# Kernel optimization log

Hardware: AMD Instinct MI355X
Metric: run time of the kernel (lower is better)

## Reference

```python
import jax, jax.numpy as jnp
import numpy as np

HEADS = 16

def _layernorm_LC(x, eps=1e-05):
    # Normalizes jointly over the last TWO dims (L, C), matching the custom LayerNorm.
    mean = jnp.mean(x, axis=(-2, -1), keepdims=True)
    var = jnp.mean((x - mean) ** 2, axis=(-2, -1), keepdims=True) + eps
    return (x - mean) / jnp.sqrt(var)  # affine is identity (ones/zeros)


def setup_inputs() -> dict:
    key = jax.random.key(0)
    ks = jax.random.split(key, 11)
    B, L, D = 2, 2048, 1024
    H = 4 * D
    s = 0.02
    return {
        'x': jax.random.normal(ks[0], (B, L, D), jnp.float32),
        'wq': jax.random.normal(ks[1], (D, D), jnp.float32) * s,
        'bq': jax.random.normal(ks[2], (D,), jnp.float32) * s,
        'wk': jax.random.normal(ks[3], (D, D), jnp.float32) * s,
        'bk': jax.random.normal(ks[4], (D,), jnp.float32) * s,
        'wv': jax.random.normal(ks[5], (D, D), jnp.float32) * s,
        'bv': jax.random.normal(ks[6], (D,), jnp.float32) * s,
        'w1': jax.random.normal(ks[7], (D, H), jnp.float32) * s,
        'b1': jax.random.normal(ks[8], (H,), jnp.float32) * s,
        'w2': jax.random.normal(ks[9], (H, D), jnp.float32) * s,
        'b2': jax.random.normal(ks[10], (D,), jnp.float32) * s,
    }


def reference(x, wq, bq, wk, bk, wv, bv, w1, b1, w2, b2):
    B, L, D = x.shape
    dh = D // HEADS
    # QKV projections
    q = (x @ wq + bq).reshape(B, L, HEADS, dh)
    k = (x @ wk + bk).reshape(B, L, HEADS, dh)
    v = (x @ wv + bv).reshape(B, L, HEADS, dh)
    # batched multi-head attention (equivalent to the per-head Python loop)
    scale = 1.0 / jnp.sqrt(jnp.float32(dh))
    scores = jnp.einsum('blhd,bmhd->bhlm', q, k) * scale
    attn = jax.nn.softmax(scores, axis=-1)
    out = jnp.einsum('bhlm,bmhd->blhd', attn, v).reshape(B, L, D)
    # residual + (L,C) layernorm
    h = _layernorm_LC(x + out)
    # feedforward (dropout is identity in eval)
    ff = jax.nn.relu(h @ w1 + b1) @ w2 + b2
    return _layernorm_LC(h + ff)
```

## Files before the change

### kernel.cpp

```cpp
#include <hip/hip_runtime.h>
#include <hip/hip_bf16.h>

typedef __hip_bfloat16 bf16;
typedef __attribute__((ext_vector_type(8))) short short8;
typedef __attribute__((ext_vector_type(4))) short short4v;
typedef __attribute__((ext_vector_type(4))) float f32x4;

#define CB 2
#define CL 2048
#define CD 1024
#define CH 4096
#define NHEADS 16
#define DH 64

__device__ __forceinline__ short f2bs(float f) {
    __hip_bfloat16 h = __float2bfloat16(f);
    return *reinterpret_cast<short*>(&h);
}
__device__ __forceinline__ float bs2f(short s) {
    __hip_bfloat16 h = *reinterpret_cast<__hip_bfloat16*>(&s);
    return __bfloat162float(h);
}

__device__ __forceinline__ void async_copy16(const short* g, short* l) {
    __builtin_amdgcn_global_load_lds((const __attribute__((address_space(1))) unsigned int*)g,
                                     (__attribute__((address_space(3))) unsigned int*)l,
                                     16, 0, 0);
}

__global__ void pack_bias_kernel(const float* __restrict__ bq, const float* __restrict__ bk,
                                 const float* __restrict__ bv, float* __restrict__ o,
                                 float* __restrict__ stats) {
    int i = blockIdx.x * 256 + threadIdx.x;
    if (i < 16) stats[i] = 0.0f;
    if (i < 3072) o[i] = i < 1024 ? bq[i] : (i < 2048 ? bk[i - 1024] : bv[i - 2048]);
}

__global__ void cvt_x_kernel(const float* __restrict__ x, short* __restrict__ o) {
    const int i = (blockIdx.x * 256 + threadIdx.x) * 4;
    const float4 v = *(const float4*)&x[i];
    short4v s; s[0] = f2bs(v.x); s[1] = f2bs(v.y); s[2] = f2bs(v.z); s[3] = f2bs(v.w);
    *(short4v*)&o[i] = s;
}

__global__ void transpose_cvt(const float* __restrict__ in, short* __restrict__ out,
                              int K, int N, int row_off) {
    __shared__ float T[32][33];
    const int tx = threadIdx.x & 31, ty = threadIdx.x >> 5;
    const int k0 = blockIdx.y * 32, n0 = blockIdx.x * 32;
    #pragma unroll
    for (int i = 0; i < 4; ++i)
        T[ty + i * 8][tx] = in[(size_t)(k0 + ty + i * 8) * N + n0 + tx];
    __syncthreads();
    #pragma unroll
    for (int i = 0; i < 4; ++i)
        out[(size_t)(row_off + n0 + ty + i * 8) * K + k0 + tx] = f2bs(T[tx][ty + i * 8]);
}

__global__ void transpose_qkv(const float* __restrict__ wq, const float* __restrict__ wk,
                              const float* __restrict__ wv, short* __restrict__ out) {
    __shared__ float T[32][33];
    const int z = blockIdx.z;
    const float* in = z == 0 ? wq : (z == 1 ? wk : wv);
    const int row_off = z * 1024;
    const int tx = threadIdx.x & 31, ty = threadIdx.x >> 5;
    const int k0 = blockIdx.y * 32, n0 = blockIdx.x * 32;
    #pragma unroll
    for (int i = 0; i < 4; ++i)
        T[ty + i * 8][tx] = in[(size_t)(k0 + ty + i * 8) * CD + n0 + tx];
    __syncthreads();
    #pragma unroll
    for (int i = 0; i < 4; ++i)
        out[(size_t)(row_off + n0 + ty + i * 8) * CD + k0 + tx] = f2bs(T[tx][ty + i * 8]);
}

template <int BN, int RELU, int EPI>
__launch_bounds__(256)
__global__ void gemm_mfma(const short* __restrict__ A,
                          const short* __restrict__ Bt,
                          const float* __restrict__ bias,
                          short* __restrict__ C,
                          short* __restrict__ C2,
                          int M, int N, int K,
                          float* __restrict__ stats) {
    constexpr int NT = BN / 32;
    __shared__ short As[128 * 32];
    __shared__ short Bs[BN * 32];
    __shared__ float red[8];

    const int tid = threadIdx.x;
    const int wave = tid >> 6, lane = tid & 63, quad = lane >> 4, lm = lane & 15;
    const int wm = (wave & 1) * 64, wn = (wave >> 1) * (NT * 16);
    const int row0 = blockIdx.y * 128, col0 = blockIdx.x * BN;

    f32x4 acc[4][NT];
    #pragma unroll
    for (int i = 0; i < 4; ++i)
        #pragma unroll
        for (int j = 0; j < NT; ++j) { f32x4 z = {0.f, 0.f, 0.f, 0.f}; acc[i][j] = z; }

    for (int k0 = 0; k0 < K; k0 += 32) {
        #pragma unroll
        for (int t = 0; t < 2; ++t) {
            int c = tid + t * 256;
            int r = c >> 2, sg = c & 3;
            async_copy16(A + (size_t)(row0 + r) * K + k0 + sg * 8, &As[c * 8]);
        }
        #pragma unroll
        for (int t = 0; t < BN / 64; ++t) {
            int c = tid + t * 256;
            int r = c >> 2, sg = c & 3;
            async_copy16(Bt + (size_t)(col0 + r) * K + k0 + sg * 8, &Bs[c * 8]);
        }
        __syncthreads();

        short8 af[4], bfr[NT];
        #pragma unroll
        for (int mt = 0; mt < 4; ++mt)
            af[mt] = *(const short8*)&As[(wm + mt * 16 + lm) * 32 + quad * 8];
        #pragma unroll
        for (int nt = 0; nt < NT; ++nt)
            bfr[nt] = *(const short8*)&Bs[(wn + nt * 16 + lm) * 32 + quad * 8];
        #pragma unroll
        for (int mt = 0; mt < 4; ++mt)
            #pragma unroll
            for (int nt = 0; nt < NT; ++nt)
                acc[mt][nt] = __builtin_amdgcn_mfma_f32_16x16x32_bf16(af[mt], bfr[nt], acc[mt][nt], 0, 0, 0);
        __syncthreads();
    }

    float s1 = 0.f, s2 = 0.f;
    #pragma unroll
    for (int mt = 0; mt < 4; ++mt) {
        #pragma unroll
        for (int nt = 0; nt < NT; ++nt) {
            const int col = col0 + wn + nt * 16 + lm;
            const float bv = bias[col];
            const int rowb = row0 + wm + mt * 16 + quad * 4;
            if (EPI == 1 && col >= 2048) {
                const int b = row0 >> 11;
                const int l0 = rowb & (CL - 1);
                short4v sv;
                #pragma unroll
                for (int r = 0; r < 4; ++r) sv[r] = f2bs(acc[mt][nt][r] + bv);
                *(short4v*)&C2[(size_t)b * CD * CL + (size_t)(col - 2048) * CL + l0] = sv;
            } else {
                #pragma unroll
                for (int r = 0; r < 4; ++r) {
                    float v = acc[mt][nt][r] + bv;
                    if (RELU) v = fmaxf(v, 0.f);
                    const int ld = (EPI == 1) ? 2048 : N;
                    const size_t idx = (size_t)(rowb + r) * ld + col;
                    if (EPI == 2) {
                        v += bs2f(C[idx]);
                        s1 += v; s2 += v * v;
                    }
                    C[idx] = f2bs(v);
                }
            }
        }
    }
    if (EPI == 2) {
        #pragma unroll
        for (int off = 1; off <= 32; off <<= 1) {
            s1 += __shfl_xor(s1, off, 64);
            s2 += __shfl_xor(s2, off, 64);
        }
        if (lane == 0) { red[wave] = s1; red[4 + wave] = s2; }
        __syncthreads();
        if (tid == 0) {
            const int batch = row0 >> 11;
            atomicAdd(&stats[batch * 2 + 0], red[0] + red[1] + red[2] + red[3]);
            atomicAdd(&stats[batch * 2 + 1], red[4] + red[5] + red[6] + red[7]);
        }
    }
}

__launch_bounds__(256)
__global__ void attn_mfma(const short* __restrict__ qk,
                          const short* __restrict__ vT,
                          const float* __restrict__ x,
                          short* __restrict__ sbuf,
                          float* __restrict__ stats) {
    __shared__ short Ks[64 * 64];
    __shared__ short Vt[64 * 66];
    __shared__ float red[8];

    const int tid = threadIdx.x;
    const int wave = tid >> 6, lane = tid & 63, quad = lane >> 4, lm = lane & 15;
    const int h = blockIdx.y, b = blockIdx.z;
    const int hoff = h * DH;
    const size_t rowb = (size_t)b * CL;
    const size_t vbase = (size_t)b * CD * CL + (size_t)hoff * CL;
    const int qbase0 = blockIdx.x * 128 + wave * 32;

    short8 bq[2][2];
    #pragma unroll
    for (int qt = 0; qt < 2; ++qt)
        #pragma unroll
        for (int kf = 0; kf < 2; ++kf)
            bq[qt][kf] = *(const short8*)(qk + (rowb + qbase0 + qt * 16 + lm) * 2048 + hoff + kf * 32 + quad * 8);

    f32x4 oacc[2][4];
    #pragma unroll
    for (int qt = 0; qt < 2; ++qt)
        #pragma unroll
        for (int mt = 0; mt < 4; ++mt) { f32x4 z = {0.f, 0.f, 0.f, 0.f}; oacc[qt][mt] = z; }
    float lsum[2] = {0.f, 0.f};

    for (int kt = 0; kt < CL / 64; ++kt) {
        #pragma unroll
        for (int t = 0; t < 2; ++t) {
            const int c = tid + t * 256;
            const int key = c >> 3, seg = c & 7;
            async_copy16(qk + (rowb + kt * 64 + key) * 2048 + 1024 + hoff + seg * 8, &Ks[c * 8]);
        }
        #pragma unroll
        for (int t = 0; t < 2; ++t) {
            const int c = tid + t * 256;
            const int row = c >> 3, seg = c & 7;
            const short8 vv = *(const short8*)(vT + vbase + (size_t)row * CL + kt * 64 + seg * 8);
            *(short8*)&Vt[row * 66 + seg * 8] = vv;
        }
        __syncthreads();

        float st[2][4][4];
        #pragma unroll
        for (int ktile = 0; ktile < 4; ++ktile) {
            const short8 a0 = *(const short8*)&Ks[(ktile * 16 + lm) * 64 + quad * 8];
            const short8 a1 = *(const short8*)&Ks[(ktile * 16 + lm) * 64 + 32 + quad * 8];
            #pragma unroll
            for (int qt = 0; qt < 2; ++qt) {
                f32x4 s = {0.f, 0.f, 0.f, 0.f};
                s = __builtin_amdgcn_mfma_f32_16x16x32_bf16(a0, bq[qt][0], s, 0, 0, 0);
                s = __builtin_amdgcn_mfma_f32_16x16x32_bf16(a1, bq[qt][1], s, 0, 0, 0);
                #pragma unroll
                for (int r = 0; r < 4; ++r) {
                    const float p = __expf(s[r] * 0.125f);
                    lsum[qt] += p;
                    st[qt][ktile][r] = p;
                }
            }
        }

        #pragma unroll
        for (int p = 0; p < 2; ++p) {
            short8 pf[2];
            #pragma unroll
            for (int qt = 0; qt < 2; ++qt)
                #pragma unroll
                for (int r = 0; r < 4; ++r) {
                    pf[qt][r]     = f2bs(st[qt][2 * p][r]);
                    pf[qt][4 + r] = f2bs(st[qt][2 * p + 1][r]);
                }
            #pragma unroll
            for (int mt = 0; mt < 4; ++mt) {
                const int vr = (mt * 16 + lm) * 66 + p * 32 + quad * 4;
                const short4v vlo = *(const short4v*)&Vt[vr];
                const short4v vhi = *(const short4v*)&Vt[vr + 16];
                short8 vf;
                vf[0] = vlo[0]; vf[1] = vlo[1]; vf[2] = vlo[2]; vf[3] = vlo[3];
                vf[4] = vhi[0]; vf[5] = vhi[1]; vf[6] = vhi[2]; vf[7] = vhi[3];
                #pragma unroll
                for (int qt = 0; qt < 2; ++qt)
                    oacc[qt][mt] = __builtin_amdgcn_mfma_f32_16x16x32_bf16(vf, pf[qt], oacc[qt][mt], 0, 0, 0);
            }
        }
        __syncthreads();
    }

    #pragma unroll
    for (int qt = 0; qt < 2; ++qt) {
        lsum[qt] += __shfl_xor(lsum[qt], 16, 64);
        lsum[qt] += __shfl_xor(lsum[qt], 32, 64);
    }

    float s1 = 0.f, s2 = 0.f;
    #pragma unroll
    for (int qt = 0; qt < 2; ++qt) {
        const float inv = 1.0f / lsum[qt];
        const size_t grow = rowb + qbase0 + qt * 16 + lm;
        #pragma unroll
        for (int mt = 0; mt < 4; ++mt) {
            const size_t base = grow * CD + hoff + mt * 16 + quad * 4;
            const float4 xv = *(const float4*)&x[base];
            const float xa[4] = {xv.x, xv.y, xv.z, xv.w};
            short4v sv;
            #pragma unroll
            for (int r = 0; r < 4; ++r) {
                const float s = xa[r] + oacc[qt][mt][r] * inv;
                s1 += s; s2 += s * s;
                sv[r] = f2bs(s);
            }
            *(short4v*)&sbuf[base] = sv;
        }
    }
    #pragma unroll
    for (int off = 1; off <= 32; off <<= 1) {
        s1 += __shfl_xor(s1, off, 64);
        s2 += __shfl_xor(s2, off, 64);
    }
    if (lane == 0) { red[wave] = s1; red[4 + wave] = s2; }
    __syncthreads();
    if (tid == 0) {
        atomicAdd(&stats[b * 2 + 0], red[0] + red[1] + red[2] + red[3]);
        atomicAdd(&stats[b * 2 + 1], red[4] + red[5] + red[6] + red[7]);
    }
}

template <typename TO>
__global__ void ln_apply(const short* __restrict__ s, const float* __restrict__ stats,
                         TO* __restrict__ out, int perBatch) {
    const int bId = blockIdx.y;
    const size_t base = (size_t)bId * perBatch;
    const float n = (float)perBatch;
    const float mean = stats[bId * 2 + 0] / n;
    const float var  = stats[bId * 2 + 1] / n - mean * mean + 1e-5f;
    const float inv  = rsqrtf(var);
    const int stride = gridDim.x * 256 * 8;
    for (int i = (blockIdx.x * 256 + threadIdx.x) * 8; i < perBatch; i += stride) {
        const short8 v8 = *(const short8*)&s[base + i];
        float o[8];
        #pragma unroll
        for (int j = 0; j < 8; ++j) o[j] = (bs2f(v8[j]) - mean) * inv;
        if (sizeof(TO) == 4) {
            float4 f0 = {o[0], o[1], o[2], o[3]}, f1 = {o[4], o[5], o[6], o[7]};
            *(float4*)&((float*)out)[base + i] = f0;
            *(float4*)&((float*)out)[base + i + 4] = f1;
        } else {
            short8 r;
            #pragma unroll
            for (int j = 0; j < 8; ++j) r[j] = f2bs(o[j]);
            *(short8*)&((short*)out)[base + i] = r;
        }
    }
}

extern "C" void kernel_launch(void* const* d_in, const int* in_sizes, int n_in,
                              void* d_out, int out_size, void* d_ws, size_t ws_size,
                              hipStream_t stream) {
    const float* x  = (const float*)d_in[0];
    const float* wq = (const float*)d_in[1];
    const float* bq = (const float*)d_in[2];
    const float* wk = (const float*)d_in[3];
    const float* bk = (const float*)d_in[4];
    const float* wv = (const float*)d_in[5];
    const float* bv = (const float*)d_in[6];
    const float* w1 = (const float*)d_in[7];
    const float* b1 = (const float*)d_in[8];
    const float* w2 = (const float*)d_in[9];
    const float* b2 = (const float*)d_in[10];

    const int BL = CB * CL;
    const int perBatch = CL * CD;

    char* ws = (char*)d_ws;
    const size_t MB = 1024 * 1024;
    short* Wqkvt = (short*)(ws);
    float* bqkv  = (float*)(ws + 6 * MB);
    short* w1t   = (short*)(ws);
    short* w2t   = (short*)(ws);
    short* xbf   = (short*)(ws + 8 * MB);
    short* qkb   = (short*)(ws + 16 * MB);
    short* vT    = (short*)(ws + 32 * MB);
    short* ff1   = (short*)(ws + 8 * MB);
    short* hbuf  = (short*)(ws + 40 * MB);
    float* stats = (float*)(ws + 48 * MB);

    dim3 blk(256);

    pack_bias_kernel<<<12, blk, 0, stream>>>(bq, bk, bv, bqkv, stats);
    cvt_x_kernel<<<BL * CD / 1024, blk, 0, stream>>>(x, xbf);
    transpose_qkv<<<dim3(32, 32, 3), blk, 0, stream>>>(wq, wk, wv, Wqkvt);

    gemm_mfma<128, 0, 1><<<dim3(3072 / 128, BL / 128), blk, 0, stream>>>(
        xbf, Wqkvt, bqkv, qkb, vT, BL, 3072, CD, nullptr);

    attn_mfma<<<dim3(CL / 128, NHEADS, CB), blk, 0, stream>>>(qkb, vT, x, hbuf, stats);

    ln_apply<bf16><<<dim3(128, CB), blk, 0, stream>>>(hbuf, stats, (bf16*)hbuf, perBatch);

    transpose_cvt<<<dim3(128, 32), blk, 0, stream>>>(w1, w1t, CD, CH, 0);
    gemm_mfma<128, 1, 0><<<dim3(CH / 128, BL / 128), blk, 0, stream>>>(
        hbuf, w1t, b1, ff1, nullptr, BL, CH, CD, nullptr);

    transpose_cvt<<<dim3(32, 128), blk, 0, stream>>>(w2, w2t, CH, CD, 0);
    gemm_mfma<64, 0, 2><<<dim3(CD / 64, BL / 128), blk, 0, stream>>>(
        ff1, w2t, b2, hbuf, nullptr, BL, CD, CH, stats + 8);

    ln_apply<float><<<dim3(128, CB), blk, 0, stream>>>(hbuf, stats + 8, (float*)d_out, perBatch);
}
```

Baseline: 387.8 us.

## Double GEMM K-step to 64 and remap blocks for XCD-local L2 reuse

The GEMM kernel now loads two 32-wide K slabs per iteration into doubled shared buffers, which halves the number of barrier pairs per K sweep. Both the GEMM and attention kernels remap the linear block id so that blocks landing on the same XCD (id mod 8) share row tiles or head/batch groups, improving L2 locality. The GEMM remap hardcodes 32 row tiles (M=4096) and the attention remap hardcodes a 16x16x2 grid, so it breaks if launch shapes differ. Doubled LDS use may also lower occupancy.

```diff
diff --git a/kernel.cpp b/kernel.cpp
--- a/kernel.cpp
+++ b/kernel.cpp
@@ -84,14 +84,19 @@
                           int M, int N, int K,
                           float* __restrict__ stats) {
     constexpr int NT = BN / 32;
-    __shared__ short As[128 * 32];
-    __shared__ short Bs[BN * 32];
+    __shared__ short As[2 * 128 * 32];
+    __shared__ short Bs[2 * BN * 32];
     __shared__ float red[8];
 
     const int tid = threadIdx.x;
     const int wave = tid >> 6, lane = tid & 63, quad = lane >> 4, lm = lane & 15;
     const int wm = (wave & 1) * 64, wn = (wave >> 1) * (NT * 16);
-    const int row0 = blockIdx.y * 128, col0 = blockIdx.x * BN;
+
+    const int id = blockIdx.y * gridDim.x + blockIdx.x;
+    const int xcd = id & 7, within = id >> 3;
+    const int by = xcd * 4 + (within & 3);
+    const int bx = within >> 2;
+    const int row0 = by * 128, col0 = bx * BN;
 
     f32x4 acc[4][NT];
     #pragma unroll
@@ -99,33 +104,38 @@
         #pragma unroll
         for (int j = 0; j < NT; ++j) { f32x4 z = {0.f, 0.f, 0.f, 0.f}; acc[i][j] = z; }
 
-    for (int k0 = 0; k0 < K; k0 += 32) {
-        #pragma unroll
-        for (int t = 0; t < 2; ++t) {
-            int c = tid + t * 256;
-            int r = c >> 2, sg = c & 3;
-            async_copy16(A + (size_t)(row0 + r) * K + k0 + sg * 8, &As[c * 8]);
-        }
-        #pragma unroll
-        for (int t = 0; t < BN / 64; ++t) {
-            int c = tid + t * 256;
-            int r = c >> 2, sg = c & 3;
-            async_copy16(Bt + (size_t)(col0 + r) * K + k0 + sg * 8, &Bs[c * 8]);
+    for (int k0 = 0; k0 < K; k0 += 64) {
+        #pragma unroll
+        for (int t = 0; t < 4; ++t) {
+            const int c = t * 256 + tid;
+            const int slab = c >> 9, idx = c & 511;
+            const int r = idx >> 2, seg = idx & 3;
+            async_copy16(A + (size_t)(row0 + r) * K + k0 + slab * 32 + seg * 8, &As[c * 8]);
+        }
+        #pragma unroll
+        for (int t = 0; t < BN / 32; ++t) {
+            const int c = t * 256 + tid;
+            const int slab = c / (BN * 4), idx = c % (BN * 4);
+            const int r = idx >> 2, seg = idx & 3;
+            async_copy16(Bt + (size_t)(col0 + r) * K + k0 + slab * 32 + seg * 8, &Bs[c * 8]);
         }
         __syncthreads();
 
-        short8 af[4], bfr[NT];
-        #pragma unroll
-        for (int mt = 0; mt < 4; ++mt)
-            af[mt] = *(const short8*)&As[(wm + mt * 16 + lm) * 32 + quad * 8];
-        #pragma unroll
-        for (int nt = 0; nt < NT; ++nt)
-            bfr[nt] = *(const short8*)&Bs[(wn + nt * 16 + lm) * 32 + quad * 8];
-        #pragma unroll
-        for (int mt = 0; mt < 4; ++mt)
+        #pragma unroll
+        for (int kh = 0; kh < 2; ++kh) {
+            short8 af[4], bfr[NT];
+            #pragma unroll
+            for (int mt = 0; mt < 4; ++mt)
+                af[mt] = *(const short8*)&As[kh * 4096 + (wm + mt * 16 + lm) * 32 + quad * 8];
             #pragma unroll
             for (int nt = 0; nt < NT; ++nt)
-                acc[mt][nt] = __builtin_amdgcn_mfma_f32_16x16x32_bf16(af[mt], bfr[nt], acc[mt][nt], 0, 0, 0);
+                bfr[nt] = *(const short8*)&Bs[kh * (BN * 32) + (wn + nt * 16 + lm) * 32 + quad * 8];
+            #pragma unroll
+            for (int mt = 0; mt < 4; ++mt)
+                #pragma unroll
+                for (int nt = 0; nt < NT; ++nt)
+                    acc[mt][nt] = __builtin_amdgcn_mfma_f32_16x16x32_bf16(af[mt], bfr[nt], acc[mt][nt], 0, 0, 0);
+        }
         __syncthreads();
     }
 
@@ -188,11 +198,17 @@
 
     const int tid = threadIdx.x;
     const int wave = tid >> 6, lane = tid & 63, quad = lane >> 4, lm = lane & 15;
-    const int h = blockIdx.y, b = blockIdx.z;
+
+    const int id = blockIdx.z * (16 * 16) + blockIdx.y * 16 + blockIdx.x;
+    const int xcd = id & 7, rest = id >> 3;
+    const int qx = rest & 15, gq = rest >> 4;
+    const int g = gq * 8 + xcd;
+    const int h = g & 15, b = g >> 4;
+
     const int hoff = h * DH;
     const size_t rowb = (size_t)b * CL;
     const size_t vbase = (size_t)b * CD * CL + (size_t)hoff * CL;
-    const int qbase0 = blockIdx.x * 128 + wave * 32;
+    const int qbase0 = qx * 128 + wave * 32;
 
     short8 bq[2][2];
     #pragma unroll
```

Measured after the change: 368.7 us. 1.05x faster.
